# Kernel optimization log

Measured on AMD Instinct MI355X. Metric: run time of the kernel, lower is better.

## Reference

```python
import jax, jax.numpy as jnp
import numpy as np

H, D_IN, D_ATT, D_OUT, S, T = 16, 1024, 64, 64, 2048, 2048


def setup_inputs() -> dict:
    key = jax.random.key(0)
    ks = jax.random.split(key, 12)
    s = lambda fan_in: 1.0 / np.sqrt(fan_in)
    inp = {
        "current_tokens": jax.random.normal(ks[0], (S, D_IN), jnp.float32),
        "context_tokens": jax.random.normal(ks[1], (T, D_IN), jnp.float32),
        # per-head projection weights (stacked over heads)
        "Wq": jax.random.uniform(ks[2], (H, D_IN, D_ATT), jnp.float32, -s(D_IN), s(D_IN)),
        "bq": jax.random.uniform(ks[3], (H, D_ATT), jnp.float32, -s(D_IN), s(D_IN)),
        "Wk": jax.random.uniform(ks[4], (H, D_IN, D_ATT), jnp.float32, -s(D_IN), s(D_IN)),
        "bk": jax.random.uniform(ks[5], (H, D_ATT), jnp.float32, -s(D_IN), s(D_IN)),
        "Wv": jax.random.uniform(ks[6], (H, D_IN, D_OUT), jnp.float32, -s(D_IN), s(D_IN)),
        "bv": jax.random.uniform(ks[7], (H, D_OUT), jnp.float32, -s(D_IN), s(D_IN)),
        # out_proj: Linear(H*D_OUT -> D_OUT)
        "Wo": jax.random.uniform(ks[8], (H * D_OUT, D_OUT), jnp.float32, -s(H * D_OUT), s(H * D_OUT)),
        "bo": jax.random.uniform(ks[9], (D_OUT,), jnp.float32, -s(H * D_OUT), s(H * D_OUT)),
    }
    return inp


def reference(current_tokens, context_tokens, Wq, bq, Wk, bk, Wv, bv, Wo, bo):
    # Batched over heads: q,k: [H,S/T,D_ATT], v: [H,T,D_OUT]
    q = jnp.einsum("si,hid->hsd", current_tokens, Wq) + bq[:, None, :]
    k = jnp.einsum("ti,hid->htd", context_tokens, Wk) + bk[:, None, :]
    v = jnp.einsum("ti,hio->hto", context_tokens, Wv) + bv[:, None, :]
    scores = jnp.einsum("hsd,htd->hst", q, k) / jnp.sqrt(jnp.asarray(D_ATT, q.dtype))
    attn = jax.nn.softmax(scores, axis=-1)          # [H,S,T]
    y = jnp.einsum("hst,hto->hso", attn, v)          # [H,S,D_OUT]
    # torch.cat(ys, dim=0) -> [H*S, D_OUT]; .view(-1, H*D_OUT) -> [S, H*D_OUT]
    # (row-major reshape of head-major stacking, exactly as the torch code does)
    y = y.reshape(-1, D_OUT).reshape(-1, H * D_OUT)
    return y @ Wo + bo                               # [S, D_OUT]
```

## Files before the change

kernel.cpp:

```cpp
#include <hip/hip_runtime.h>

#define DEV static __device__ __forceinline__

typedef unsigned short u16;
typedef unsigned int u32;
typedef float f32x4 __attribute__((ext_vector_type(4)));
typedef __bf16 bf16x8 __attribute__((ext_vector_type(8)));
typedef unsigned short u16x8 __attribute__((ext_vector_type(8)));
typedef unsigned int u32x2 __attribute__((ext_vector_type(2)));
typedef unsigned int u32x4 __attribute__((ext_vector_type(4)));

constexpr int H = 16, DIN = 1024, DH = 64, S = 2048, T = 2048;
constexpr float SM_C = 0.18033688011112042f;

DEV u16 f2bf(float f) { return __builtin_bit_cast(u16, (__bf16)f); }
DEV float bf2f(u16 u) { u32 i = (u32)u << 16; return __builtin_bit_cast(float, i); }
DEV bf16x8 ld_bf8(const u16* p) { return __builtin_bit_cast(bf16x8, *(const u16x8*)p); }
DEV u32 cvtpk(float lo, float hi) {
  u32 r; asm("v_cvt_pk_bf16_f32 %0, %1, %2" : "=v"(r) : "v"(lo), "v"(hi)); return r;
}

#define GLOAD16(gp, lp) __builtin_amdgcn_global_load_lds( \
    (const __attribute__((address_space(1))) void*)(gp),  \
    (__attribute__((address_space(3))) void*)(lp), 16, 0, 0)

__global__ __launch_bounds__(256) void cvt_kernel(const float* __restrict__ a,
                                                  const float* __restrict__ b,
                                                  u16* __restrict__ oa, u16* __restrict__ ob) {
  int i = blockIdx.x * 256 + threadIdx.x;
  const float* in; u16* out; int j;
  if (i < 262144) { in = a; out = oa; j = i; }
  else            { in = b; out = ob; j = i - 262144; }
  const float4* p = (const float4*)(in + (size_t)j * 8);
  float4 x = p[0], y = p[1];
  u16x8 o;
  o[0] = f2bf(x.x); o[1] = f2bf(x.y); o[2] = f2bf(x.z); o[3] = f2bf(x.w);
  o[4] = f2bf(y.x); o[5] = f2bf(y.y); o[6] = f2bf(y.z); o[7] = f2bf(y.w);
  *(u16x8*)(out + (size_t)j * 8) = o;
}

__global__ __launch_bounds__(256) void twp_all_kernel(
    const float* __restrict__ Wq, const float* __restrict__ Wk,
    const float* __restrict__ Wv, const float* __restrict__ Wo,
    u16* __restrict__ WqT, u16* __restrict__ WkvT, u16* __restrict__ WoT) {
  int y = blockIdx.y, k0 = blockIdx.x * 64;
  const float* W; u16* Wt; float scale = 1.0f;
  if (y < 16)      { W = Wq + (size_t)y * DIN * DH;        Wt = WqT + (size_t)y * DH * DIN; scale = SM_C; }
  else if (y < 32) { W = Wk + (size_t)(y - 16) * DIN * DH; Wt = WkvT + (size_t)(y - 16) * DH * DIN; }
  else if (y < 48) { W = Wv + (size_t)(y - 32) * DIN * DH; Wt = WkvT + (size_t)(y - 16) * DH * DIN; }
  else             { W = Wo;                               Wt = WoT; }
  __shared__ alignas(16) float tile[64 * 68];
  int tid = threadIdx.x;
#pragma unroll
  for (int it = 0; it < 4; ++it) {
    int slot = it * 256 + tid;
    int i = slot >> 4, j4 = (slot & 15) * 4;
    *(float4*)&tile[i * 68 + j4] = *(const float4*)&W[(size_t)(k0 + i) * 64 + j4];
  }
  __syncthreads();
  int n = tid >> 2, kb = (tid & 3) * 16;
  u16x8 o0, o1;
#pragma unroll
  for (int j = 0; j < 8; ++j) o0[j] = f2bf(tile[(kb + j) * 68 + n] * scale);
#pragma unroll
  for (int j = 0; j < 8; ++j) o1[j] = f2bf(tile[(kb + 8 + j) * 68 + n] * scale);
  *(u16x8*)&Wt[(size_t)n * DIN + k0 + kb] = o0;
  *(u16x8*)&Wt[(size_t)n * DIN + k0 + kb + 8] = o1;
}

__global__ __launch_bounds__(256) void gemm_qkv_kernel(
    const u16* __restrict__ Acur, const u16* __restrict__ Actx,
    const u16* __restrict__ WqT, const u16* __restrict__ WkvT,
    const float* __restrict__ bq, const float* __restrict__ bk, const float* __restrict__ bv,
    u16* __restrict__ Qall, u16* __restrict__ Kall, u16* __restrict__ Vall) {
  __shared__ alignas(16) u16 As[2][128 * 64];
  __shared__ alignas(16) u16 Bs[2][64 * 64];
  int bid = blockIdx.x;
  const u16 *A, *W; const float* bias; u16* dst; int m0, n0, nc0; float bscale = 1.0f;
  if (bid < 256) {
    A = Acur; W = WqT; bias = bq; dst = Qall; bscale = SM_C;
    m0 = (bid >> 4) * 128; n0 = (bid & 15) * 64; nc0 = n0;
  } else {
    int b2 = bid - 256;
    A = Actx; W = WkvT;
    m0 = (b2 >> 5) * 128; n0 = (b2 & 31) * 64;
    if (n0 < 1024) { bias = bk; dst = Kall; nc0 = n0; }
    else           { bias = bv; dst = Vall; nc0 = n0 - 1024; }
  }
  int tid = threadIdx.x, w = tid >> 6, l = tid & 63, g = l >> 4, r = l & 15;
  auto stage = [&](int buf, int kt) {
#pragma unroll
    for (int it = 0; it < 4; ++it) {
      int c = it * 256 + tid, row = c >> 3, q = c & 7;
      GLOAD16(&A[(size_t)(m0 + row) * DIN + kt + ((q ^ (row & 7)) << 3)], &As[buf][c * 8]);
    }
#pragma unroll
    for (int it = 0; it < 2; ++it) {
      int c = it * 256 + tid, row = c >> 3, q = c & 7;
      GLOAD16(&W[(size_t)(n0 + row) * DIN + kt + ((q ^ (row & 7)) << 3)], &Bs[buf][c * 8]);
    }
  };
  stage(0, 0);
  __syncthreads();
  f32x4 acc[2][4] = {};
  for (int t = 0; t < 16; ++t) {
    if (t < 15) stage((t + 1) & 1, (t + 1) * 64);
    int cur = t & 1;
#pragma unroll
    for (int kk = 0; kk < 2; ++kk) {
      int qo = (((kk << 2) | g) ^ (r & 7)) << 3;
      bf16x8 a0 = ld_bf8(&As[cur][(w * 32 + r) * 64 + qo]);
      bf16x8 a1 = ld_bf8(&As[cur][(w * 32 + 16 + r) * 64 + qo]);
#pragma unroll
      for (int nf = 0; nf < 4; ++nf) {
        bf16x8 b = ld_bf8(&Bs[cur][(nf * 16 + r) * 64 + qo]);
        acc[0][nf] = __builtin_amdgcn_mfma_f32_16x16x32_bf16(a0, b, acc[0][nf], 0, 0, 0);
        acc[1][nf] = __builtin_amdgcn_mfma_f32_16x16x32_bf16(a1, b, acc[1][nf], 0, 0, 0);
      }
    }
    __syncthreads();
  }
#pragma unroll
  for (int mi = 0; mi < 2; ++mi)
#pragma unroll
    for (int nf = 0; nf < 4; ++nf)
#pragma unroll
      for (int rr = 0; rr < 4; ++rr) {
        int row = m0 + w * 32 + mi * 16 + 4 * g + rr, col = nc0 + nf * 16 + r;
        dst[(size_t)row * 1024 + col] = f2bf(acc[mi][nf][rr] + bias[col] * bscale);
      }
}

__global__ __launch_bounds__(256) void vtrans_kernel(const u16* __restrict__ Vall,
                                                     u16* __restrict__ VtAll) {
  int t0 = blockIdx.x * 64, d0 = blockIdx.y * 64;
  __shared__ alignas(16) u16 tile[64 * 72];
  int tid = threadIdx.x;
#pragma unroll
  for (int it = 0; it < 2; ++it) {
    int c = it * 256 + tid, trow = c >> 3, u = (c & 7) * 8;
    *(u16x8*)&tile[trow * 72 + u] = *(const u16x8*)&Vall[(size_t)(t0 + trow) * 1024 + d0 + u];
  }
  __syncthreads();
#pragma unroll
  for (int it = 0; it < 2; ++it) {
    int c = it * 256 + tid, drow = c >> 3, u = (c & 7) * 8;
    u16x8 o;
#pragma unroll
    for (int e = 0; e < 8; ++e) o[e] = tile[(u + e) * 72 + drow];
    *(u16x8*)&VtAll[(size_t)(d0 + drow) * 2048 + t0 + u] = o;
  }
}

__global__ __launch_bounds__(256) void attn_kernel(
    const u16* __restrict__ Qall, const u16* __restrict__ Kall,
    const u16* __restrict__ VtAll, u16* __restrict__ OPa, u16* __restrict__ OPb,
    float* __restrict__ LP) {
  int qb = blockIdx.x, h = blockIdx.y, ts = blockIdx.z;
  int tid = threadIdx.x, w = tid >> 6, l = tid & 63, g = l >> 4, r = l & 15;
  __shared__ alignas(16) u16 Ks[2][64 * 64];
  __shared__ alignas(16) u16 Vs[2][64 * 64];
  const int q0 = qb * 128 + w * 32;
  bf16x8 qf[2][2];
#pragma unroll
  for (int sub = 0; sub < 2; ++sub)
#pragma unroll
    for (int kk = 0; kk < 2; ++kk)
      qf[sub][kk] = ld_bf8(&Qall[(size_t)(q0 + sub * 16 + r) * 1024 + h * 64 + kk * 32 + 8 * g]);
  f32x4 o[2][4] = {};
  float lsum[2] = {0.f, 0.f};
  const int tBeg = ts * 512, tEnd = tBeg + 512;

  auto stage = [&](int buf, int t0) {
#pragma unroll
    for (int it = 0; it < 2; ++it) {
      int c = it * 256 + tid, row = c >> 3, q = c & 7;
      int qs = (q ^ (row & 7)) << 3;
      GLOAD16(&Kall[(size_t)(t0 + row) * 1024 + h * 64 + qs], &Ks[buf][c * 8]);
      GLOAD16(&VtAll[(size_t)(h * 64 + row) * 2048 + t0 + qs], &Vs[buf][c * 8]);
    }
  };
  stage(0, tBeg);
  __syncthreads();
  int cur = 0;
  for (int t0 = tBeg; t0 < tEnd; t0 += 64) {
    if (t0 + 64 < tEnd) stage(cur ^ 1, t0 + 64);
    f32x4 sacc[2][4] = {};
#pragma unroll
    for (int kk = 0; kk < 2; ++kk) {
      int qo = (((kk << 2) | g) ^ (r & 7)) << 3;
#pragma unroll
      for (int nf = 0; nf < 4; ++nf) {
        bf16x8 kf = ld_bf8(&Ks[cur][(nf * 16 + r) * 64 + qo]);
        sacc[0][nf] = __builtin_amdgcn_mfma_f32_16x16x32_bf16(kf, qf[0][kk], sacc[0][nf], 0, 0, 0);
        sacc[1][nf] = __builtin_amdgcn_mfma_f32_16x16x32_bf16(kf, qf[1][kk], sacc[1][nf], 0, 0, 0);
      }
    }
    u32 c[2][4][2];
#pragma unroll
    for (int sub = 0; sub < 2; ++sub)
#pragma unroll
      for (int nf = 0; nf < 4; ++nf) {
        float p0 = __builtin_amdgcn_exp2f(sacc[sub][nf][0]);
        float p1 = __builtin_amdgcn_exp2f(sacc[sub][nf][1]);
        float p2 = __builtin_amdgcn_exp2f(sacc[sub][nf][2]);
        float p3 = __builtin_amdgcn_exp2f(sacc[sub][nf][3]);
        lsum[sub] += (p0 + p1) + (p2 + p3);
        c[sub][nf][0] = cvtpk(p0, p1);
        c[sub][nf][1] = cvtpk(p2, p3);
      }
#pragma unroll
    for (int kk = 0; kk < 2; ++kk) {
      bf16x8 pB[2];
#pragma unroll
      for (int sub = 0; sub < 2; ++sub) {
        u32 dw[4];
#pragma unroll
        for (int s2 = 0; s2 < 2; ++s2) {
          u32x2 t1 = __builtin_amdgcn_permlane32_swap(c[sub][2 * kk][s2], c[sub][2 * kk + 1][s2],
                                                      false, false);
          u32x2 t2 = __builtin_amdgcn_permlane16_swap(t1.x, t1.y, false, false);
          dw[s2] = t2.x; dw[2 + s2] = t2.y;
        }
        pB[sub] = __builtin_bit_cast(bf16x8, (u32x4){dw[0], dw[1], dw[2], dw[3]});
      }
      int qo = (((kk << 2) | g) ^ (r & 7)) << 3;
#pragma unroll
      for (int nf = 0; nf < 4; ++nf) {
        bf16x8 vf = ld_bf8(&Vs[cur][(nf * 16 + r) * 64 + qo]);
        o[0][nf] = __builtin_amdgcn_mfma_f32_16x16x32_bf16(vf, pB[0], o[0][nf], 0, 0, 0);
        o[1][nf] = __builtin_amdgcn_mfma_f32_16x16x32_bf16(vf, pB[1], o[1][nf], 0, 0, 0);
      }
    }
    __syncthreads();
    cur ^= 1;
  }
  u16* op = (ts == 3) ? OPb : OPa + (size_t)ts * (16 * 2048 * 64);
#pragma unroll
  for (int sub = 0; sub < 2; ++sub) {
    float ls = lsum[sub];
    ls += __shfl_xor(ls, 16, 64);
    ls += __shfl_xor(ls, 32, 64);
    int s = q0 + sub * 16 + r;
    if (l < 16) LP[(size_t)(ts * 16 + h) * 2048 + s] = ls;
#pragma unroll
    for (int nf = 0; nf < 4; ++nf) {
      uint2 pd;
      pd.x = cvtpk(o[sub][nf][0], o[sub][nf][1]);
      pd.y = cvtpk(o[sub][nf][2], o[sub][nf][3]);
      *(uint2*)&op[((size_t)h * 2048 + s) * 64 + nf * 16 + 4 * g] = pd;
    }
  }
}

__global__ __launch_bounds__(256) void combine_kernel(const u16* __restrict__ OPa,
                                                      const u16* __restrict__ OPb,
                                                      const float* __restrict__ LP,
                                                      u16* __restrict__ G) {
  int j = blockIdx.x * 256 + threadIdx.x;
  int base = j * 8;
  int d = base & 63, s = (base >> 6) & 2047, h = base >> 17;
  float acc[8] = {};
  float lsum = 0.f;
#pragma unroll
  for (int ts = 0; ts < 4; ++ts) {
    const u16* op = (ts == 3) ? OPb : OPa + (size_t)ts * (16 * 2048 * 64);
    u16x8 v = *(const u16x8*)&op[((size_t)h * 2048 + s) * 64 + d];
#pragma unroll
    for (int e = 0; e < 8; ++e) acc[e] += bf2f(v[e]);
    lsum += LP[(size_t)(ts * 16 + h) * 2048 + s];
  }
  float inv = 1.0f / lsum;
  u16x8 out;
#pragma unroll
  for (int e = 0; e < 8; ++e) out[e] = f2bf(acc[e] * inv);
  *(u16x8*)&G[(size_t)(h * 128 + (s >> 4)) * 1024 + (s & 15) * 64 + d] = out;
}

__global__ __launch_bounds__(256) void oproj_part_kernel(const u16* __restrict__ G,
                                                         const u16* __restrict__ WoT,
                                                         float* __restrict__ Part) {
  __shared__ alignas(16) u16 As[128 * 64];
  __shared__ alignas(16) u16 Bs[64 * 64];
  int m0 = blockIdx.x * 128, kz = blockIdx.y;
  int tid = threadIdx.x, w = tid >> 6, l = tid & 63, g = l >> 4, r = l & 15;
  f32x4 acc[2][4] = {};
  for (int ks = 0; ks < 2; ++ks) {
    int kt = kz * 128 + ks * 64;
#pragma unroll
    for (int it = 0; it < 4; ++it) {
      int c = it * 256 + tid, row = c >> 3, q = c & 7;
      GLOAD16(&G[(size_t)(m0 + row) * DIN + kt + ((q ^ (row & 7)) << 3)], &As[c * 8]);
    }
#pragma unroll
    for (int it = 0; it < 2; ++it) {
      int c = it * 256 + tid, row = c >> 3, q = c & 7;
      GLOAD16(&WoT[(size_t)row * DIN + kt + ((q ^ (row & 7)) << 3)], &Bs[c * 8]);
    }
    __syncthreads();
#pragma unroll
    for (int kk = 0; kk < 2; ++kk) {
      int qo = (((kk << 2) | g) ^ (r & 7)) << 3;
      bf16x8 a0 = ld_bf8(&As[(w * 32 + r) * 64 + qo]);
      bf16x8 a1 = ld_bf8(&As[(w * 32 + 16 + r) * 64 + qo]);
#pragma unroll
      for (int nf = 0; nf < 4; ++nf) {
        bf16x8 b = ld_bf8(&Bs[(nf * 16 + r) * 64 + qo]);
        acc[0][nf] = __builtin_amdgcn_mfma_f32_16x16x32_bf16(a0, b, acc[0][nf], 0, 0, 0);
        acc[1][nf] = __builtin_amdgcn_mfma_f32_16x16x32_bf16(a1, b, acc[1][nf], 0, 0, 0);
      }
    }
    __syncthreads();
  }
#pragma unroll
  for (int mi = 0; mi < 2; ++mi)
#pragma unroll
    for (int nf = 0; nf < 4; ++nf)
#pragma unroll
      for (int rr = 0; rr < 4; ++rr)
        Part[((size_t)kz * 2048 + m0 + w * 32 + mi * 16 + 4 * g + rr) * 64 + nf * 16 + r] =
            acc[mi][nf][rr];
}

__global__ __launch_bounds__(256) void oproj_reduce_kernel(const float* __restrict__ Part,
                                                           const float* __restrict__ bo,
                                                           float* __restrict__ out) {
  int i = blockIdx.x * 256 + threadIdx.x;
  float s = bo[i & 63];
#pragma unroll
  for (int kz = 0; kz < 8; ++kz) s += Part[(size_t)kz * 131072 + i];
  out[i] = s;
}

extern "C" void kernel_launch(void* const* d_in, const int* in_sizes, int n_in,
                              void* d_out, int out_size, void* d_ws, size_t ws_size,
                              hipStream_t stream) {
  const float* cur = (const float*)d_in[0];
  const float* ctx = (const float*)d_in[1];
  const float* Wq = (const float*)d_in[2];
  const float* bq = (const float*)d_in[3];
  const float* Wk = (const float*)d_in[4];
  const float* bk = (const float*)d_in[5];
  const float* Wv = (const float*)d_in[6];
  const float* bv = (const float*)d_in[7];
  const float* Wo = (const float*)d_in[8];
  const float* bo = (const float*)d_in[9];
  float* out = (float*)d_out;

  char* ws = (char*)d_ws;
  const size_t MB = 1ull << 20;
  u16* cur_bf = (u16*)(ws + 0 * MB);
  u16* ctx_bf = (u16*)(ws + 4 * MB);
  u16* WqT    = (u16*)(ws + 8 * MB);
  u16* WkvT   = (u16*)(ws + 10 * MB);
  u16* Qall   = (u16*)(ws + 14 * MB);
  u16* Kall   = (u16*)(ws + 18 * MB);
  u16* Vall   = (u16*)(ws + 22 * MB);
  u16* VtAll  = (u16*)(ws + 26 * MB);
  u16* WoT    = (u16*)(ws + 30 * MB);
  u16* OPa    = (u16*)(ws + 0 * MB);
  u16* OPb    = (u16*)(ws + 22 * MB);
  float* LP   = (float*)(ws + 12 * MB);
  u16* G      = (u16*)(ws + 14 * MB);
  float* Part = (float*)(ws + 18 * MB);

  cvt_kernel<<<2048, 256, 0, stream>>>(cur, ctx, cur_bf, ctx_bf);
  twp_all_kernel<<<dim3(16, 49), 256, 0, stream>>>(Wq, Wk, Wv, Wo, WqT, WkvT, WoT);
  gemm_qkv_kernel<<<768, 256, 0, stream>>>(cur_bf, ctx_bf, WqT, WkvT, bq, bk, bv,
                                           Qall, Kall, Vall);
  vtrans_kernel<<<dim3(32, 16), 256, 0, stream>>>(Vall, VtAll);
  attn_kernel<<<dim3(16, 16, 4), 256, 0, stream>>>(Qall, Kall, VtAll, OPa, OPb, LP);
  combine_kernel<<<1024, 256, 0, stream>>>(OPa, OPb, LP, G);
  oproj_part_kernel<<<dim3(16, 8), 256, 0, stream>>>(G, WoT, Part);
  oproj_reduce_kernel<<<512, 256, 0, stream>>>(Part, bo, out);
}
```

Before: 79.29 us.

## Fuse prep kernels, fold V transpose into QKV GEMM, enlarge GEMM and attention tiles

Merges the input cast and weight-transpose kernels into a single launch. Removes the separate V transpose kernel: the QKV GEMM computes V blocks with swapped MFMA operands and writes V transposed directly. The QKV GEMM now uses 128x128 tiles with a 2x2 warp layout. The attention kernel now handles 256 query rows per block, so each K/V tile is reused across more queries. Together these cut launches and intermediate traffic, at the cost of higher register pressure, fewer attention blocks, and an extra barrier per k-step in the GEMM.

```diff
diff --git a/kernel.cpp b/kernel.cpp
--- a/kernel.cpp
+++ b/kernel.cpp
@@ -24,33 +24,33 @@
     (const __attribute__((address_space(1))) void*)(gp),  \
     (__attribute__((address_space(3))) void*)(lp), 16, 0, 0)
 
-__global__ __launch_bounds__(256) void cvt_kernel(const float* __restrict__ a,
-                                                  const float* __restrict__ b,
-                                                  u16* __restrict__ oa, u16* __restrict__ ob) {
-  int i = blockIdx.x * 256 + threadIdx.x;
-  const float* in; u16* out; int j;
-  if (i < 262144) { in = a; out = oa; j = i; }
-  else            { in = b; out = ob; j = i - 262144; }
-  const float4* p = (const float4*)(in + (size_t)j * 8);
-  float4 x = p[0], y = p[1];
-  u16x8 o;
-  o[0] = f2bf(x.x); o[1] = f2bf(x.y); o[2] = f2bf(x.z); o[3] = f2bf(x.w);
-  o[4] = f2bf(y.x); o[5] = f2bf(y.y); o[6] = f2bf(y.z); o[7] = f2bf(y.w);
-  *(u16x8*)(out + (size_t)j * 8) = o;
-}
-
-__global__ __launch_bounds__(256) void twp_all_kernel(
+__global__ __launch_bounds__(256) void prep_kernel(
+    const float* __restrict__ cur, const float* __restrict__ ctx,
     const float* __restrict__ Wq, const float* __restrict__ Wk,
     const float* __restrict__ Wv, const float* __restrict__ Wo,
+    u16* __restrict__ cur_bf, u16* __restrict__ ctx_bf,
     u16* __restrict__ WqT, u16* __restrict__ WkvT, u16* __restrict__ WoT) {
-  int y = blockIdx.y, k0 = blockIdx.x * 64;
+  __shared__ alignas(16) float tile[64 * 68];
+  int bid = blockIdx.x, tid = threadIdx.x;
+  if (bid < 2048) {
+    int i = bid * 256 + tid;
+    const float* in; u16* out; int j;
+    if (i < 262144) { in = cur; out = cur_bf; j = i; }
+    else            { in = ctx; out = ctx_bf; j = i - 262144; }
+    const float4* p = (const float4*)(in + (size_t)j * 8);
+    float4 x = p[0], y = p[1];
+    u16x8 o;
+    o[0] = f2bf(x.x); o[1] = f2bf(x.y); o[2] = f2bf(x.z); o[3] = f2bf(x.w);
+    o[4] = f2bf(y.x); o[5] = f2bf(y.y); o[6] = f2bf(y.z); o[7] = f2bf(y.w);
+    *(u16x8*)(out + (size_t)j * 8) = o;
+    return;
+  }
+  int t = bid - 2048, k0 = (t & 15) * 64, y = t >> 4;
   const float* W; u16* Wt; float scale = 1.0f;
   if (y < 16)      { W = Wq + (size_t)y * DIN * DH;        Wt = WqT + (size_t)y * DH * DIN; scale = SM_C; }
   else if (y < 32) { W = Wk + (size_t)(y - 16) * DIN * DH; Wt = WkvT + (size_t)(y - 16) * DH * DIN; }
   else if (y < 48) { W = Wv + (size_t)(y - 32) * DIN * DH; Wt = WkvT + (size_t)(y - 16) * DH * DIN; }
   else             { W = Wo;                               Wt = WoT; }
-  __shared__ alignas(16) float tile[64 * 68];
-  int tid = threadIdx.x;
 #pragma unroll
   for (int it = 0; it < 4; ++it) {
     int slot = it * 256 + tid;
@@ -72,22 +72,20 @@
     const u16* __restrict__ Acur, const u16* __restrict__ Actx,
     const u16* __restrict__ WqT, const u16* __restrict__ WkvT,
     const float* __restrict__ bq, const float* __restrict__ bk, const float* __restrict__ bv,
-    u16* __restrict__ Qall, u16* __restrict__ Kall, u16* __restrict__ Vall) {
+    u16* __restrict__ Qall, u16* __restrict__ Kall, u16* __restrict__ VtAll) {
   __shared__ alignas(16) u16 As[2][128 * 64];
-  __shared__ alignas(16) u16 Bs[2][64 * 64];
+  __shared__ alignas(16) u16 Bs[2][128 * 64];
   int bid = blockIdx.x;
-  const u16 *A, *W; const float* bias; u16* dst; int m0, n0, nc0; float bscale = 1.0f;
-  if (bid < 256) {
-    A = Acur; W = WqT; bias = bq; dst = Qall; bscale = SM_C;
-    m0 = (bid >> 4) * 128; n0 = (bid & 15) * 64; nc0 = n0;
-  } else {
-    int b2 = bid - 256;
-    A = Actx; W = WkvT;
-    m0 = (b2 >> 5) * 128; n0 = (b2 & 31) * 64;
-    if (n0 < 1024) { bias = bk; dst = Kall; nc0 = n0; }
-    else           { bias = bv; dst = Vall; nc0 = n0 - 1024; }
-  }
+  const u16 *A, *W; int m0, n0, mode;
+  if (bid < 128) { A = Acur; W = WqT; m0 = (bid >> 3) * 128; n0 = (bid & 7) * 128; mode = 0; }
+  else {
+    int b2 = bid - 128;
+    A = Actx; W = WkvT; m0 = (b2 >> 4) * 128; n0 = (b2 & 15) * 128;
+    mode = (n0 < 1024) ? 1 : 2;
+  }
+  int nc0 = (mode == 2) ? n0 - 1024 : n0;
   int tid = threadIdx.x, w = tid >> 6, l = tid & 63, g = l >> 4, r = l & 15;
+  int wr = w >> 1, wc = w & 1;
   auto stage = [&](int buf, int kt) {
 #pragma unroll
     for (int it = 0; it < 4; ++it) {
@@ -95,80 +93,83 @@
       GLOAD16(&A[(size_t)(m0 + row) * DIN + kt + ((q ^ (row & 7)) << 3)], &As[buf][c * 8]);
     }
 #pragma unroll
-    for (int it = 0; it < 2; ++it) {
+    for (int it = 0; it < 4; ++it) {
       int c = it * 256 + tid, row = c >> 3, q = c & 7;
       GLOAD16(&W[(size_t)(n0 + row) * DIN + kt + ((q ^ (row & 7)) << 3)], &Bs[buf][c * 8]);
     }
   };
   stage(0, 0);
   __syncthreads();
-  f32x4 acc[2][4] = {};
+  f32x4 acc[4][4] = {};
   for (int t = 0; t < 16; ++t) {
     if (t < 15) stage((t + 1) & 1, (t + 1) * 64);
     int cur = t & 1;
 #pragma unroll
     for (int kk = 0; kk < 2; ++kk) {
       int qo = (((kk << 2) | g) ^ (r & 7)) << 3;
-      bf16x8 a0 = ld_bf8(&As[cur][(w * 32 + r) * 64 + qo]);
-      bf16x8 a1 = ld_bf8(&As[cur][(w * 32 + 16 + r) * 64 + qo]);
-#pragma unroll
-      for (int nf = 0; nf < 4; ++nf) {
-        bf16x8 b = ld_bf8(&Bs[cur][(nf * 16 + r) * 64 + qo]);
-        acc[0][nf] = __builtin_amdgcn_mfma_f32_16x16x32_bf16(a0, b, acc[0][nf], 0, 0, 0);
-        acc[1][nf] = __builtin_amdgcn_mfma_f32_16x16x32_bf16(a1, b, acc[1][nf], 0, 0, 0);
-      }
-    }
-    __syncthreads();
-  }
-#pragma unroll
-  for (int mi = 0; mi < 2; ++mi)
-#pragma unroll
-    for (int nf = 0; nf < 4; ++nf)
-#pragma unroll
-      for (int rr = 0; rr < 4; ++rr) {
-        int row = m0 + w * 32 + mi * 16 + 4 * g + rr, col = nc0 + nf * 16 + r;
-        dst[(size_t)row * 1024 + col] = f2bf(acc[mi][nf][rr] + bias[col] * bscale);
-      }
-}
-
-__global__ __launch_bounds__(256) void vtrans_kernel(const u16* __restrict__ Vall,
-                                                     u16* __restrict__ VtAll) {
-  int t0 = blockIdx.x * 64, d0 = blockIdx.y * 64;
-  __shared__ alignas(16) u16 tile[64 * 72];
-  int tid = threadIdx.x;
-#pragma unroll
-  for (int it = 0; it < 2; ++it) {
-    int c = it * 256 + tid, trow = c >> 3, u = (c & 7) * 8;
-    *(u16x8*)&tile[trow * 72 + u] = *(const u16x8*)&Vall[(size_t)(t0 + trow) * 1024 + d0 + u];
-  }
-  __syncthreads();
-#pragma unroll
-  for (int it = 0; it < 2; ++it) {
-    int c = it * 256 + tid, drow = c >> 3, u = (c & 7) * 8;
-    u16x8 o;
-#pragma unroll
-    for (int e = 0; e < 8; ++e) o[e] = tile[(u + e) * 72 + drow];
-    *(u16x8*)&VtAll[(size_t)(d0 + drow) * 2048 + t0 + u] = o;
-  }
-}
-
-__global__ __launch_bounds__(256) void attn_kernel(
+      bf16x8 av[4], bv2[4];
+#pragma unroll
+      for (int mi = 0; mi < 4; ++mi) av[mi] = ld_bf8(&As[cur][(wr * 64 + mi * 16 + r) * 64 + qo]);
+#pragma unroll
+      for (int nf = 0; nf < 4; ++nf) bv2[nf] = ld_bf8(&Bs[cur][(wc * 64 + nf * 16 + r) * 64 + qo]);
+      if (mode < 2) {
+#pragma unroll
+        for (int mi = 0; mi < 4; ++mi)
+#pragma unroll
+          for (int nf = 0; nf < 4; ++nf)
+            acc[mi][nf] = __builtin_amdgcn_mfma_f32_16x16x32_bf16(av[mi], bv2[nf], acc[mi][nf], 0, 0, 0);
+      } else {
+#pragma unroll
+        for (int mi = 0; mi < 4; ++mi)
+#pragma unroll
+          for (int nf = 0; nf < 4; ++nf)
+            acc[mi][nf] = __builtin_amdgcn_mfma_f32_16x16x32_bf16(bv2[nf], av[mi], acc[mi][nf], 0, 0, 0);
+      }
+      __syncthreads();
+    }
+  }
+  if (mode < 2) {
+    u16* dst = (mode == 0) ? Qall : Kall;
+    const float* bias = (mode == 0) ? bq : bk;
+    float bscale = (mode == 0) ? SM_C : 1.0f;
+#pragma unroll
+    for (int mi = 0; mi < 4; ++mi)
+#pragma unroll
+      for (int nf = 0; nf < 4; ++nf)
+#pragma unroll
+        for (int rr = 0; rr < 4; ++rr) {
+          int row = m0 + wr * 64 + mi * 16 + 4 * g + rr, col = nc0 + wc * 64 + nf * 16 + r;
+          dst[(size_t)row * 1024 + col] = f2bf(acc[mi][nf][rr] + bias[col] * bscale);
+        }
+  } else {
+#pragma unroll
+    for (int mi = 0; mi < 4; ++mi)
+#pragma unroll
+      for (int nf = 0; nf < 4; ++nf)
+#pragma unroll
+        for (int rr = 0; rr < 4; ++rr) {
+          int d = nc0 + wc * 64 + nf * 16 + 4 * g + rr, tok = m0 + wr * 64 + mi * 16 + r;
+          VtAll[(size_t)d * 2048 + tok] = f2bf(acc[mi][nf][rr] + bv[d]);
+        }
+  }
+}
+
+__global__ __launch_bounds__(256, 2) void attn_kernel(
     const u16* __restrict__ Qall, const u16* __restrict__ Kall,
-    const u16* __restrict__ VtAll, u16* __restrict__ OPa, u16* __restrict__ OPb,
-    float* __restrict__ LP) {
+    const u16* __restrict__ VtAll, u16* __restrict__ OP, float* __restrict__ LP) {
   int qb = blockIdx.x, h = blockIdx.y, ts = blockIdx.z;
   int tid = threadIdx.x, w = tid >> 6, l = tid & 63, g = l >> 4, r = l & 15;
   __shared__ alignas(16) u16 Ks[2][64 * 64];
   __shared__ alignas(16) u16 Vs[2][64 * 64];
-  const int q0 = qb * 128 + w * 32;
-  bf16x8 qf[2][2];
-#pragma unroll
-  for (int sub = 0; sub < 2; ++sub)
+  const int q0 = qb * 256 + w * 64;
+  bf16x8 qf[4][2];
+#pragma unroll
+  for (int sub = 0; sub < 4; ++sub)
 #pragma unroll
     for (int kk = 0; kk < 2; ++kk)
       qf[sub][kk] = ld_bf8(&Qall[(size_t)(q0 + sub * 16 + r) * 1024 + h * 64 + kk * 32 + 8 * g]);
-  f32x4 o[2][4] = {};
-  float lsum[2] = {0.f, 0.f};
+  f32x4 o[4][4] = {};
+  float lsum[4] = {0.f, 0.f, 0.f, 0.f};
   const int tBeg = ts * 512, tEnd = tBeg + 512;
 
   auto stage = [&](int buf, int t0) {
@@ -185,20 +186,21 @@
   int cur = 0;
   for (int t0 = tBeg; t0 < tEnd; t0 += 64) {
     if (t0 + 64 < tEnd) stage(cur ^ 1, t0 + 64);
-    f32x4 sacc[2][4] = {};
+    f32x4 sacc[4][4] = {};
 #pragma unroll
     for (int kk = 0; kk < 2; ++kk) {
       int qo = (((kk << 2) | g) ^ (r & 7)) << 3;
 #pragma unroll
       for (int nf = 0; nf < 4; ++nf) {
         bf16x8 kf = ld_bf8(&Ks[cur][(nf * 16 + r) * 64 + qo]);
-        sacc[0][nf] = __builtin_amdgcn_mfma_f32_16x16x32_bf16(kf, qf[0][kk], sacc[0][nf], 0, 0, 0);
-        sacc[1][nf] = __builtin_amdgcn_mfma_f32_16x16x32_bf16(kf, qf[1][kk], sacc[1][nf], 0, 0, 0);
-      }
-    }
-    u32 c[2][4][2];
-#pragma unroll
-    for (int sub = 0; sub < 2; ++sub)
+#pragma unroll
+        for (int sub = 0; sub < 4; ++sub)
+          sacc[sub][nf] = __builtin_amdgcn_mfma_f32_16x16x32_bf16(kf, qf[sub][kk], sacc[sub][nf], 0, 0, 0);
+      }
+    }
+    u32 c[4][4][2];
+#pragma unroll
+    for (int sub = 0; sub < 4; ++sub)
 #pragma unroll
       for (int nf = 0; nf < 4; ++nf) {
         float p0 = __builtin_amdgcn_exp2f(sacc[sub][nf][0]);
@@ -211,9 +213,12 @@
       }
 #pragma unroll
     for (int kk = 0; kk < 2; ++kk) {
-      bf16x8 pB[2];
-#pragma unroll
-      for (int sub = 0; sub < 2; ++sub) {
+      int qo = (((kk << 2) | g) ^ (r & 7)) << 3;
+      bf16x8 vf[4];
+#pragma unroll
+      for (int nf = 0; nf < 4; ++nf) vf[nf] = ld_bf8(&Vs[cur][(nf * 16 + r) * 64 + qo]);
+#pragma unroll
+      for (int sub = 0; sub < 4; ++sub) {
         u32 dw[4];
 #pragma unroll
         for (int s2 = 0; s2 < 2; ++s2) {
@@ -222,22 +227,17 @@
           u32x2 t2 = __builtin_amdgcn_permlane16_swap(t1.x, t1.y, false, false);
           dw[s2] = t2.x; dw[2 + s2] = t2.y;
         }
-        pB[sub] = __builtin_bit_cast(bf16x8, (u32x4){dw[0], dw[1], dw[2], dw[3]});
-      }
-      int qo = (((kk << 2) | g) ^ (r & 7)) << 3;
-#pragma unroll
-      for (int nf = 0; nf < 4; ++nf) {
-        bf16x8 vf = ld_bf8(&Vs[cur][(nf * 16 + r) * 64 + qo]);
-        o[0][nf] = __builtin_amdgcn_mfma_f32_16x16x32_bf16(vf, pB[0], o[0][nf], 0, 0, 0);
-        o[1][nf] = __builtin_amdgcn_mfma_f32_16x16x32_bf16(vf, pB[1], o[1][nf], 0, 0, 0);
+        bf16x8 pB = __builtin_bit_cast(bf16x8, (u32x4){dw[0], dw[1], dw[2], dw[3]});
+#pragma unroll
+        for (int nf = 0; nf < 4; ++nf)
+          o[sub][nf] = __builtin_amdgcn_mfma_f32_16x16x32_bf16(vf[nf], pB, o[sub][nf], 0, 0, 0);
       }
     }
     __syncthreads();
     cur ^= 1;
   }
-  u16* op = (ts == 3) ? OPb : OPa + (size_t)ts * (16 * 2048 * 64);
-#pragma unroll
-  for (int sub = 0; sub < 2; ++sub) {
+#pragma unroll
+  for (int sub = 0; sub < 4; ++sub) {
     float ls = lsum[sub];
     ls += __shfl_xor(ls, 16, 64);
     ls += __shfl_xor(ls, 32, 64);
@@ -248,13 +248,12 @@
       uint2 pd;
       pd.x = cvtpk(o[sub][nf][0], o[sub][nf][1]);
       pd.y = cvtpk(o[sub][nf][2], o[sub][nf][3]);
-      *(uint2*)&op[((size_t)h * 2048 + s) * 64 + nf * 16 + 4 * g] = pd;
-    }
-  }
-}
-
-__global__ __launch_bounds__(256) void combine_kernel(const u16* __restrict__ OPa,
-                                                      const u16* __restrict__ OPb,
+      *(uint2*)&OP[((size_t)(ts * 16 + h) * 2048 + s) * 64 + nf * 16 + 4 * g] = pd;
+    }
+  }
+}
+
+__global__ __launch_bounds__(256) void combine_kernel(const u16* __restrict__ OP,
                                                       const float* __restrict__ LP,
                                                       u16* __restrict__ G) {
   int j = blockIdx.x * 256 + threadIdx.x;
@@ -264,8 +263,7 @@
   float lsum = 0.f;
 #pragma unroll
   for (int ts = 0; ts < 4; ++ts) {
-    const u16* op = (ts == 3) ? OPb : OPa + (size_t)ts * (16 * 2048 * 64);
-    u16x8 v = *(const u16x8*)&op[((size_t)h * 2048 + s) * 64 + d];
+    u16x8 v = *(const u16x8*)&OP[((size_t)(ts * 16 + h) * 2048 + s) * 64 + d];
 #pragma unroll
     for (int e = 0; e < 8; ++e) acc[e] += bf2f(v[e]);
     lsum += LP[(size_t)(ts * 16 + h) * 2048 + s];
@@ -353,24 +351,21 @@
   u16* ctx_bf = (u16*)(ws + 4 * MB);
   u16* WqT    = (u16*)(ws + 8 * MB);
   u16* WkvT   = (u16*)(ws + 10 * MB);
-  u16* Qall   = (u16*)(ws + 14 * MB);
-  u16* Kall   = (u16*)(ws + 18 * MB);
-  u16* Vall   = (u16*)(ws + 22 * MB);
-  u16* VtAll  = (u16*)(ws + 26 * MB);
-  u16* WoT    = (u16*)(ws + 30 * MB);
-  u16* OPa    = (u16*)(ws + 0 * MB);
-  u16* OPb    = (u16*)(ws + 22 * MB);
-  float* LP   = (float*)(ws + 12 * MB);
-  u16* G      = (u16*)(ws + 14 * MB);
-  float* Part = (float*)(ws + 18 * MB);
-
-  cvt_kernel<<<2048, 256, 0, stream>>>(cur, ctx, cur_bf, ctx_bf);
-  twp_all_kernel<<<dim3(16, 49), 256, 0, stream>>>(Wq, Wk, Wv, Wo, WqT, WkvT, WoT);
-  gemm_qkv_kernel<<<768, 256, 0, stream>>>(cur_bf, ctx_bf, WqT, WkvT, bq, bk, bv,
-                                           Qall, Kall, Vall);
-  vtrans_kernel<<<dim3(32, 16), 256, 0, stream>>>(Vall, VtAll);
-  attn_kernel<<<dim3(16, 16, 4), 256, 0, stream>>>(Qall, Kall, VtAll, OPa, OPb, LP);
-  combine_kernel<<<1024, 256, 0, stream>>>(OPa, OPb, LP, G);
+  u16* WoT    = (u16*)(ws + 14 * MB);
+  u16* Qall   = (u16*)(ws + 15 * MB);
+  u16* Kall   = (u16*)(ws + 19 * MB);
+  u16* VtAll  = (u16*)(ws + 23 * MB);
+  u16* OP     = (u16*)(ws + 27 * MB);
+  float* LP   = (float*)(ws + 43 * MB);
+  u16* G      = (u16*)(ws + 44 * MB);
+  float* Part = (float*)(ws + 48 * MB);
+
+  prep_kernel<<<2832, 256, 0, stream>>>(cur, ctx, Wq, Wk, Wv, Wo, cur_bf, ctx_bf,
+                                        WqT, WkvT, WoT);
+  gemm_qkv_kernel<<<384, 256, 0, stream>>>(cur_bf, ctx_bf, WqT, WkvT, bq, bk, bv,
+                                           Qall, Kall, VtAll);
+  attn_kernel<<<dim3(8, 16, 4), 256, 0, stream>>>(Qall, Kall, VtAll, OP, LP);
+  combine_kernel<<<1024, 256, 0, stream>>>(OP, LP, G);
   oproj_part_kernel<<<dim3(16, 8), 256, 0, stream>>>(G, WoT, Part);
   oproj_reduce_kernel<<<512, 256, 0, stream>>>(Part, bo, out);
 }
```

Result: slower. 87.29 us (+10.1%).
